# Optimization experiments

Measured on AMD Instinct MI355X. Metric: run time of the kernel, lower is better.

The kernel has to match this reference:

```python
import jax, jax.numpy as jnp
import numpy as np

H, HD, NKV = 16, 128, 4           # heads, head_dim, n_kv_heads (kv_groups=4)
SEL_TOPK, SEL_DIM, SEL_HEADS = 64, 64, 1
ROPE_BASE = 10000.0


def _rope_emb(t, hd):
    inv = 1.0 / (ROPE_BASE ** (jnp.arange(0, hd, 2, dtype=jnp.float32) / hd))
    freqs = jnp.arange(t, dtype=jnp.float32)[:, None] * inv[None, :]
    return jnp.concatenate([freqs, freqs], axis=-1)  # [t, hd]


def _apply_rotary(x, rope):
    # x: [b, t, h, hd]; rope: [t, hd] (rot_dim == hd here)
    cos = jnp.cos(rope)[None, :, None, :]
    sin = jnp.sin(rope)[None, :, None, :]
    x1, x2 = x[..., ::2], x[..., 1::2]
    c, s = cos[..., ::2], sin[..., ::2]
    rot = jnp.stack([x1 * c - x2 * s, x1 * s + x2 * c], axis=-1)
    return rot.reshape(x.shape)


def _selector_mask(q, k):
    # q, k: [b, H, t, hd] in UNrotated form (selector_rope='none'); causal=True
    b, h, t, d = q.shape
    qs = q[:, :SEL_HEADS, :, :SEL_DIM]
    ks = k[:, :SEL_HEADS, :, :SEL_DIM]
    scores = jnp.einsum('bhqd,bhkd->bhqk', qs, ks) / np.sqrt(SEL_DIM).astype(np.float32)
    future = jnp.triu(jnp.ones((t, t), bool), 1)
    scores = jnp.where(future[None, None], -jnp.inf, scores)
    idx = jax.lax.top_k(scores, SEL_TOPK)[1]  # [b, h_sel, t, keep]
    rows = jnp.arange(t)
    scatter_row = lambda im: jnp.zeros((t, t), bool).at[rows[:, None], im].set(True)
    sel = jax.vmap(jax.vmap(scatter_row))(idx)          # [b, h_sel, t, t]
    sel = sel.at[:, :, rows, rows].set(True)            # diagonal always kept
    sel = sel & jnp.tril(jnp.ones((t, t), bool))[None, None]
    sel = jnp.any(sel, axis=1, keepdims=True)           # h_sel < h -> broadcast mask
    return jnp.where(sel, 0.0, -jnp.inf).astype(jnp.float32)


def reference(x, Wq, bq, Wkd, bkd, Wku, bku, Wo, bo):
    b, t, d = x.shape
    G = H // NKV
    q = (x @ Wq + bq).reshape(b, t, H, HD)
    kv = (x @ Wkd + bkd) @ Wku + bku                    # MLA: down then up projection
    k = kv[..., : NKV * HD].reshape(b, t, NKV, HD)
    v = kv[..., NKV * HD:].reshape(b, t, NKV, HD)
    rope = _rope_emb(t, HD)
    qb = _apply_rotary(q, rope).transpose(0, 2, 1, 3)                     # [b,H,t,hd]
    kb = jnp.repeat(_apply_rotary(k, rope).transpose(0, 2, 1, 3), G, 1)   # GQA expand
    vb = jnp.repeat(v.transpose(0, 2, 1, 3), G, 1)
    # selector mask from unrotated q/k, detached (selector_detach=True)
    qu = jax.lax.stop_gradient(q.transpose(0, 2, 1, 3))
    ku = jnp.repeat(jax.lax.stop_gradient(k.transpose(0, 2, 1, 3)), G, 1)
    mask = _selector_mask(qu, ku)                                         # [b,1,t,t]
    scores = jnp.einsum('bhqd,bhkd->bhqk', qb, kb) / np.sqrt(HD).astype(np.float32)
    attn = jax.nn.softmax(scores + mask, axis=-1)
    y = jnp.einsum('bhqk,bhkd->bhqd', attn, vb)
    y = y.transpose(0, 2, 1, 3).reshape(b, t, H * HD)
    return y @ Wo + bo


def setup_inputs() -> dict:
    key = jax.random.key(0)
    ks = jax.random.split(key, 6)
    B, T, D, LAT = 2, 2048, 2048, 512
    s = 0.02
    return {
        'x': jax.random.normal(ks[0], (B, T, D), jnp.float32),
        'Wq': jax.random.normal(ks[1], (D, H * HD), jnp.float32) * s,
        'bq': jnp.zeros((H * HD,), jnp.float32),
        'Wkd': jax.random.normal(ks[2], (D, LAT), jnp.float32) * s,
        'bkd': jnp.zeros((LAT,), jnp.float32),
        'Wku': jax.random.normal(ks[3], (LAT, 2 * NKV * HD), jnp.float32) * s,
        'bku': jnp.zeros((2 * NKV * HD,), jnp.float32),
        'Wo': jax.random.normal(ks[4], (H * HD, D), jnp.float32) * s,
        'bo': jnp.zeros((D,), jnp.float32),
    }
```

## Files before the change

kernel.cpp:

```cpp
#include <hip/hip_runtime.h>

typedef unsigned int u32;
typedef unsigned long long u64;
typedef _Float16 f16;
typedef __attribute__((ext_vector_type(2))) _Float16 f16x2;
typedef __attribute__((ext_vector_type(4))) _Float16 f16x4;
typedef __attribute__((ext_vector_type(8))) _Float16 f16x8;
typedef __attribute__((ext_vector_type(4))) float f32x4;
typedef __attribute__((ext_vector_type(2))) double f64x2;


__device__ __forceinline__ int suX(int jj) { return jj ^ ((jj >> 4) & 7); }

__global__ __launch_bounds__(256) void k_transpose_cast(const float* __restrict__ in,
                                                        f16* __restrict__ out, int R, int C)
{
  __shared__ float tile[32][33];
  int c0 = blockIdx.x * 32, r0 = blockIdx.y * 32;
  int tx = threadIdx.x & 31, ty = threadIdx.x >> 5;
  #pragma unroll
  for (int i = ty; i < 32; i += 8) tile[i][tx] = in[(size_t)(r0 + i) * C + c0 + tx];
  __syncthreads();
  #pragma unroll
  for (int i = ty; i < 32; i += 8) out[(size_t)(c0 + i) * R + r0 + tx] = (f16)tile[tx][i];
}

__global__ __launch_bounds__(256) void k_cast_f16(const float* __restrict__ in,
                                                  f16* __restrict__ out, int n4)
{
  int i = blockIdx.x * 256 + threadIdx.x;
  if (i >= n4) return;
  f32x4 v = *(const f32x4*)&in[(size_t)i * 4];
  f16x4 h; h.x = (f16)v.x; h.y = (f16)v.y; h.z = (f16)v.z; h.w = (f16)v.w;
  *(f16x4*)&out[(size_t)i * 4] = h;
}

__global__ void k_prep_sel(const float* __restrict__ Wq, const float* __restrict__ Wkd,
                           const float* __restrict__ Wku, double* __restrict__ Bsel)
{
  const int k = blockIdx.x;
  const int j = threadIdx.x;
  Bsel[(size_t)k * 128 + j] = (double)Wq[(size_t)k * 2048 + j];
  double s = 0.0;
  for (int l = 0; l < 512; ++l)
    s = fma((double)Wkd[(size_t)k * 512 + l], (double)Wku[(size_t)l * 1024 + j], s);
  Bsel[(size_t)k * 128 + 64 + j] = s;
}

__global__ void k_bias_sel(const float* __restrict__ bq, const float* __restrict__ bkd,
                           const float* __restrict__ Wku, const float* __restrict__ bku,
                           double* __restrict__ bsel)
{
  int j = threadIdx.x;
  if (j < 64) {
    bsel[j] = (double)bq[j];
  } else {
    int jj = j - 64;
    double s = (double)bku[jj];
    for (int l = 0; l < 512; ++l)
      s = fma((double)bkd[l], (double)Wku[(size_t)l * 1024 + jj], s);
    bsel[j] = s;
  }
}

__global__ __launch_bounds__(256) void k_gemm_sel_f64(const float* __restrict__ A,
                                                      const double* __restrict__ Bsel,
                                                      double* __restrict__ partial)
{
  __shared__ double As[32][33];
  __shared__ double Bs[32][66];
  const int m0 = blockIdx.x * 32, n0 = blockIdx.y * 64;
  const int kbase = blockIdx.z * 512, kend = kbase + 512;
  const int tid = threadIdx.x;
  const int tx = tid & 15, ty = tid >> 4;
  const int ar = tid >> 3, ac4 = (tid & 7) * 4;
  double acc[2][4] = {};

  f32x4 aN = *(const f32x4*)&A[(size_t)(m0 + ar) * 2048 + kbase + ac4];
  f64x2 bN[4];
  #pragma unroll
  for (int it = 0; it < 4; ++it) {
    int c = it * 256 + tid; int kk = c >> 5, n2 = (c & 31) * 2;
    bN[it] = *(const f64x2*)&Bsel[(size_t)(kbase + kk) * 128 + n0 + n2];
  }
  for (int k0 = kbase; k0 < kend; k0 += 32) {
    __syncthreads();
    As[ar][ac4] = (double)aN.x; As[ar][ac4 + 1] = (double)aN.y;
    As[ar][ac4 + 2] = (double)aN.z; As[ar][ac4 + 3] = (double)aN.w;
    #pragma unroll
    for (int it = 0; it < 4; ++it) {
      int c = it * 256 + tid; int kk = c >> 5, n2 = (c & 31) * 2;
      Bs[kk][n2] = bN[it].x; Bs[kk][n2 + 1] = bN[it].y;
    }
    __syncthreads();
    if (k0 + 32 < kend) {
      aN = *(const f32x4*)&A[(size_t)(m0 + ar) * 2048 + k0 + 32 + ac4];
      #pragma unroll
      for (int it = 0; it < 4; ++it) {
        int c = it * 256 + tid; int kk = c >> 5, n2 = (c & 31) * 2;
        bN[it] = *(const f64x2*)&Bsel[(size_t)(k0 + 32 + kk) * 128 + n0 + n2];
      }
    }
    #pragma unroll
    for (int kk = 0; kk < 32; ++kk) {
      double a0 = As[ty * 2][kk], a1 = As[ty * 2 + 1][kk];
      f64x2 b01 = *(const f64x2*)&Bs[kk][tx * 4];
      f64x2 b23 = *(const f64x2*)&Bs[kk][tx * 4 + 2];
      acc[0][0] = fma(a0, b01.x, acc[0][0]); acc[0][1] = fma(a0, b01.y, acc[0][1]);
      acc[0][2] = fma(a0, b23.x, acc[0][2]); acc[0][3] = fma(a0, b23.y, acc[0][3]);
      acc[1][0] = fma(a1, b01.x, acc[1][0]); acc[1][1] = fma(a1, b01.y, acc[1][1]);
      acc[1][2] = fma(a1, b23.x, acc[1][2]); acc[1][3] = fma(a1, b23.y, acc[1][3]);
    }
  }
  double* op = partial + (size_t)blockIdx.z * 4096 * 128;
  #pragma unroll
  for (int i = 0; i < 2; ++i) {
    int row = m0 + ty * 2 + i;
    #pragma unroll
    for (int j = 0; j < 4; ++j) {
      int n = n0 + tx * 4 + j;
      op[(size_t)row * 128 + n] = acc[i][j];
    }
  }
}

__global__ __launch_bounds__(256) void k_sel_reduce(const double* __restrict__ partial,
                                                    const double* __restrict__ bias,
                                                    double* __restrict__ qs64,
                                                    double* __restrict__ ks64)
{
  const int idx = blockIdx.x * 256 + threadIdx.x;
  const int row = idx >> 7, n = idx & 127;
  const size_t S = 4096 * 128;
  double v = ((partial[idx] + partial[S + idx]) + partial[2 * S + idx]) + partial[3 * S + idx];
  v += bias[n];
  if (n < 64) qs64[(size_t)row * 64 + n] = v;
  else        ks64[(size_t)row * 64 + (n - 64)] = v;
}

__global__ __launch_bounds__(256) void k_transpose64(const double* __restrict__ in,
                                                     double* __restrict__ out)
{
  __shared__ double tile[32][33];
  const int bt = blockIdx.z;
  const int c0 = blockIdx.x * 32;
  const int r0 = blockIdx.y * 32;
  int tx = threadIdx.x & 31, ty = threadIdx.x >> 5;
  const double* ip = in + (size_t)bt * 2048 * 64;
  double* op = out + (size_t)bt * 64 * 2048;
  #pragma unroll
  for (int i = ty; i < 32; i += 8) tile[i][tx] = ip[(size_t)(r0 + i) * 64 + c0 + tx];
  __syncthreads();
  #pragma unroll
  for (int i = ty; i < 32; i += 8) op[(size_t)(c0 + i) * 2048 + r0 + tx] = tile[tx][i];
}

template <bool OUTF16>
__global__ __launch_bounds__(256) void k_gemm_bt(const f16* __restrict__ A,
                                                 const f16* __restrict__ BT,
                                                 const float* __restrict__ bias,
                                                 float* __restrict__ C, f16* __restrict__ Ch,
                                                 int M, int N, int K, int lda, int ldb, int ldc)
{
  __shared__ __align__(16) f16 As[128 * 64];
  __shared__ __align__(16) f16 Bs[128 * 64];
  const int tid = threadIdx.x;
  const int lane = tid & 63;
  const int wave = tid >> 6;
  int bx = blockIdx.x, by = blockIdx.y;
  {
    const int nwg = gridDim.x * gridDim.y;
    if ((nwg & 7) == 0) {
      const int bid = by * gridDim.x + bx;
      const int cpx = nwg >> 3;
      const int sbid = (bid & 7) * cpx + (bid >> 3);
      bx = sbid % gridDim.x;
      by = sbid / gridDim.x;
    }
  }
  const int m0 = bx * 128, n0 = by * 128;
  const int wr = (wave >> 1) * 64, wc = (wave & 1) * 64;
  const int lrow = lane & 15;
  const int kgrp = (lane >> 4) * 8;
  f32x4 acc[4][4] = {};

  for (int k0 = 0; k0 < K; k0 += 64) {
    __syncthreads();
    #pragma unroll
    for (int it = 0; it < 4; ++it) {
      int c = it * 256 + tid;
      int r = c >> 3, c8 = (c & 7) * 8;
      int lbase = (it * 256 + (tid & 192)) * 8;
      const f16* ga = A + (size_t)(m0 + r) * lda + k0 + c8;
      __builtin_amdgcn_global_load_lds((const __attribute__((address_space(1))) u32*)ga,
                                       (__attribute__((address_space(3))) u32*)&As[lbase],
                                       16, 0, 0);
      const f16* gb = BT + (size_t)(n0 + r) * ldb + k0 + c8;
      __builtin_amdgcn_global_load_lds((const __attribute__((address_space(1))) u32*)gb,
                                       (__attribute__((address_space(3))) u32*)&Bs[lbase],
                                       16, 0, 0);
    }
    __syncthreads();
    #pragma unroll
    for (int ks = 0; ks < 2; ++ks) {
      f16x8 af[4], bfr[4];
      #pragma unroll
      for (int m = 0; m < 4; ++m)
        af[m] = *(const f16x8*)&As[(wr + m * 16 + lrow) * 64 + ks * 32 + kgrp];
      #pragma unroll
      for (int n = 0; n < 4; ++n)
        bfr[n] = *(const f16x8*)&Bs[(wc + n * 16 + lrow) * 64 + ks * 32 + kgrp];
      #pragma unroll
      for (int m = 0; m < 4; ++m)
        #pragma unroll
        for (int n = 0; n < 4; ++n)
          acc[m][n] = __builtin_amdgcn_mfma_f32_16x16x32_f16(af[m], bfr[n], acc[m][n], 0, 0, 0);
    }
  }
  const int rbase = m0 + wr + (lane >> 4) * 4;
  #pragma unroll
  for (int n = 0; n < 4; ++n) {
    int col = n0 + wc + n * 16 + lrow;
    float bv = bias ? bias[col] : 0.0f;
    #pragma unroll
    for (int m = 0; m < 4; ++m) {
      #pragma unroll
      for (int j = 0; j < 4; ++j) {
        int rowi = rbase + m * 16 + j;
        float v = acc[m][n][j] + bv;
        if (OUTF16) Ch[(size_t)rowi * ldc + col] = (f16)v;
        else        C[(size_t)rowi * ldc + col] = v;
      }
    }
  }
}

__global__ void k_rope_table(float* __restrict__ rc, float* __restrict__ rs)
{
  int t = blockIdx.x, i = threadIdx.x;
  int fi = (2 * i) & 63;
  double inv = pow(10000.0, -(double)fi / 64.0);
  double a = (double)t * inv;
  rc[t * 64 + i] = (float)cos(a);
  rs[t * 64 + i] = (float)sin(a);
}

__global__ __launch_bounds__(256) void k_rope_q(const f16* __restrict__ q,
                                                const float* __restrict__ rc,
                                                const float* __restrict__ rs,
                                                f16* __restrict__ out)
{
  int g = blockIdx.x * 256 + threadIdx.x;
  int row = g >> 10, rem = g & 1023;
  int h = rem >> 6, i = rem & 63;
  int t = row & 2047;
  size_t base = (size_t)row * 2048 + h * 128 + 2 * i;
  f16x2 v = *(const f16x2*)&q[base];
  float x1 = (float)v.x, x2 = (float)v.y;
  float c = rc[t * 64 + i], s = rs[t * 64 + i];
  f16x2 o; o.x = (f16)(x1 * c - x2 * s); o.y = (f16)(x1 * s + x2 * c);
  *(f16x2*)&out[base] = o;
}

__global__ __launch_bounds__(256) void k_rope_kv(const f16* __restrict__ kv,
                                                 const float* __restrict__ rc,
                                                 const float* __restrict__ rs,
                                                 f16* __restrict__ kout, f16* __restrict__ vout)
{
  int g = blockIdx.x * 256 + threadIdx.x;
  int row = g >> 8, rem = g & 255;
  int kvh = rem >> 6, i = rem & 63;
  int t = row & 2047;
  size_t kb = (size_t)row * 1024 + kvh * 128 + 2 * i;
  f16x2 kvp = *(const f16x2*)&kv[kb];
  float x1 = (float)kvp.x, x2 = (float)kvp.y;
  float c = rc[t * 64 + i], s = rs[t * 64 + i];
  size_t ob = (size_t)row * 512 + kvh * 128 + 2 * i;
  f16x2 ko; ko.x = (f16)(x1 * c - x2 * s); ko.y = (f16)(x1 * s + x2 * c);
  *(f16x2*)&kout[ob] = ko;
  f16x2 vp = *(const f16x2*)&kv[(size_t)row * 1024 + 512 + kvh * 128 + 2 * i];
  *(f16x2*)&vout[ob] = vp;
}

__global__ __launch_bounds__(256) void k_topk64(const double* __restrict__ qs,
                                                const double* __restrict__ ksT,
                                                int* __restrict__ selcnt,
                                                int* __restrict__ selidx)
{
  const int r0 = blockIdx.x * 2;
  const int b = r0 >> 11;
  const int t0 = r0 & 2047, t1 = t0 + 1;
  const int tid = threadIdx.x;
  if (t1 < 64) {
    for (int lr = 0; lr < 2; ++lr) {
      int t = t0 + lr;
      int* outp = selidx + (size_t)(r0 + lr) * 68;
      for (int jj = tid; jj <= t; jj += 256) outp[jj] = jj;
      if (tid == 0) selcnt[r0 + lr] = t + 1;
    }
    return;
  }
  __shared__ double qrowP[64][2];
  __shared__ u64 su[2][2048];
  __shared__ unsigned hist[256], sA[256], sB[256];
  __shared__ unsigned s_bsel, s_larger, s_cnt;
  __shared__ u64 s_thr;
  __shared__ int s_remfin;
  __shared__ int cand[128];
  __shared__ u64 ckey[128];

  if (tid < 128) qrowP[tid >> 1][tid & 1] = qs[(size_t)(r0 + (tid & 1)) * 64 + (tid >> 1)];
  __syncthreads();
  {
    const double* kb = ksT + (size_t)b * 64 * 2048;
    const int emax = t1 >> 8;
    for (int e = 0; e <= emax; ++e) {
      const int jj = e * 256 + tid;
      double acc0 = 0.0, acc1 = 0.0;
      const double* kp = kb + jj;
      #pragma unroll 16
      for (int d = 0; d < 64; ++d) {
        double kv = kp[(size_t)d * 2048];
        f64x2 qp = *(const f64x2*)&qrowP[d][0];
        acc0 = fma(qp.x, kv, acc0);
        acc1 = fma(qp.y, kv, acc1);
      }
      const int sx = suX(jj);
      u64 u0 = (u64)__double_as_longlong(acc0);
      su[0][sx] = (u0 >> 63) ? ~u0 : (u0 | 0x8000000000000000ull);
      u64 u1 = (u64)__double_as_longlong(acc1);
      su[1][sx] = (u1 >> 63) ? ~u1 : (u1 | 0x8000000000000000ull);
    }
  }
  __syncthreads();

  const int c0 = tid * 8;
  for (int lr = 0; lr < 2; ++lr) {
    const int t = t0 + lr;
    int* outp = selidx + (size_t)(r0 + lr) * 68;
    const u64* S = su[lr];
    u64 prefix = 0;
    int remaining = 64;
    int broke = 0, sh_final = 0;
    for (int byte = 7; byte >= 0; --byte) {
      const int sh = byte * 8;
      hist[tid] = 0;
      __syncthreads();
      {
        unsigned bn[8]; bool vl[8];
        #pragma unroll
        for (int e = 0; e < 8; ++e) {
          int jj = c0 + e;
          u64 u = (jj <= t) ? S[suX(jj)] : 0;
          bool ok = (jj <= t) && ((byte == 7) || (((u ^ prefix) >> (sh + 8)) == 0));
          bn[e] = (unsigned)((u >> sh) & 255);
          vl[e] = ok;
        }
        #pragma unroll
        for (int e = 0; e < 8; ++e) {
          if (vl[e]) {
            bool first = true;
            #pragma unroll
            for (int p = 0; p < 8; ++p)
              if (p < e && vl[p] && bn[p] == bn[e]) first = false;
            if (first) {
              unsigned c = 0;
              #pragma unroll
              for (int q = 0; q < 8; ++q)
                if (q >= e && vl[q] && bn[q] == bn[e]) ++c;
              atomicAdd(&hist[bn[e]], c);
            }
          }
        }
      }
      __syncthreads();
      unsigned* sp = sA; unsigned* dp = sB;
      sp[tid] = hist[tid];
      __syncthreads();
      #pragma unroll
      for (int off = 1; off < 256; off <<= 1) {
        dp[tid] = sp[tid] + ((tid + off < 256) ? sp[tid + off] : 0u);
        __syncthreads();
        unsigned* tpp = sp; sp = dp; dp = tpp;
      }
      unsigned inc = sp[tid];
      unsigned cumAbove = (tid == 255) ? 0u : sp[tid + 1];
      if ((int)cumAbove < remaining && (int)inc >= remaining) {
        s_bsel = (unsigned)tid;
        s_larger = cumAbove;
        s_cnt = inc - cumAbove;
      }
      __syncthreads();
      prefix |= ((u64)s_bsel << sh);
      remaining -= (int)s_larger;
      int cnt = (int)s_cnt;
      __syncthreads();
      if (cnt <= 128) { broke = 1; sh_final = sh; break; }
    }
    u64 thr;
    int remfin;
    if (broke) {
      unsigned cg = 0;
      #pragma unroll
      for (int e = 0; e < 8; ++e) {
        int jj = c0 + e;
        if (jj <= t && (((S[suX(jj)] ^ prefix) >> sh_final) == 0)) ++cg;
      }
      unsigned* sp = sA; unsigned* dp = sB;
      sp[tid] = cg;
      __syncthreads();
      #pragma unroll
      for (int off = 1; off < 256; off <<= 1) {
        dp[tid] = sp[tid] + ((tid >= off) ? sp[tid - off] : 0u);
        __syncthreads();
        unsigned* tpp = sp; sp = dp; dp = tpp;
      }
      const int C = (int)sp[255];
      int pos = (int)(sp[tid] - cg);
      #pragma unroll
      for (int e = 0; e < 8; ++e) {
        int jj = c0 + e;
        if (jj <= t && (((S[suX(jj)] ^ prefix) >> sh_final) == 0)) cand[pos++] = jj;
      }
      __syncthreads();
      if (tid < C) ckey[tid] = S[suX(cand[tid])];
      __syncthreads();
      if (tid < C) {
        u64 k = ckey[tid];
        int g = 0, eq = 0;
        for (int j = 0; j < C; ++j) {
          g += (ckey[j] > k) ? 1 : 0;
          eq += (ckey[j] == k) ? 1 : 0;
        }
        if (g < remaining && remaining <= g + eq) {
          s_thr = k;
          s_remfin = remaining - g;
        }
      }
      __syncthreads();
      thr = s_thr;
      remfin = s_remfin;
    } else {
      thr = prefix;
      remfin = remaining;
    }
    __syncthreads();
    unsigned cg = 0, ct_ = 0;
    #pragma unroll
    for (int e = 0; e < 8; ++e) {
      int jj = c0 + e;
      if (jj <= t) {
        u64 u = S[suX(jj)];
        cg += (u > thr) ? 1u : 0u;
        ct_ += (u == thr) ? 1u : 0u;
      }
    }
    const unsigned pack = cg | (ct_ << 16);
    {
      unsigned* sp = sA; unsigned* dp = sB;
      sp[tid] = pack;
      __syncthreads();
      #pragma unroll
      for (int off = 1; off < 256; off <<= 1) {
        dp[tid] = sp[tid] + ((tid >= off) ? sp[tid - off] : 0u);
        __syncthreads();
        unsigned* tpp = sp; sp = dp; dp = tpp;
      }
      const unsigned excl = sp[tid] - pack;
      const unsigned tot = sp[255];
      const unsigned Gtot = tot & 0xFFFFu;
      const u64 ut = S[suX(t)];
      const unsigned gt = (ut > thr) ? 1u : 0u;
      const unsigned tt = (ut == thr) ? 1u : 0u;
      const int GtotX = (int)(Gtot - gt);
      int gpos = (int)(excl & 0xFFFFu);
      int tpos = (int)(excl >> 16);
      #pragma unroll
      for (int e = 0; e < 8; ++e) {
        int jj = c0 + e;
        if (jj > t) break;
        u64 u = S[suX(jj)];
        if (u > thr) {
          if (jj != t) outp[1 + gpos] = jj;
          ++gpos;
        } else if (u == thr) {
          if (jj != t && tpos < remfin) outp[1 + GtotX + tpos] = jj;
          ++tpos;
        }
      }
      if (tid == 0) {
        outp[0] = t;
        const unsigned Ttot = tot >> 16;
        int tb = (int)(Ttot - tt);
        int emitT = tb < remfin ? tb : remfin;
        selcnt[r0 + lr] = 1 + GtotX + emitT;
      }
    }
    __syncthreads();
  }
}

__global__ __launch_bounds__(256) void k_attn(const f16* __restrict__ qr,
                                              const f16* __restrict__ kr,
                                              const f16* __restrict__ vv,
                                              const int* __restrict__ selcnt,
                                              const int* __restrict__ selidx,
                                              f16* __restrict__ y)
{
  const int blk = blockIdx.x;
  const int row = blk >> 2, kvh = blk & 3;
  const int b = row >> 11;
  const int tid = threadIdx.x, lane = tid & 63, wave = tid >> 6;
  const int cnt = selcnt[row];
  __shared__ int sidx[68];
  __shared__ __align__(16) f16 Kl[65 * 128];
  __shared__ __align__(16) f16 Vl[68 * 128];
  __shared__ f16 qlds[4][128];
  __shared__ __align__(16) float pl[4][68];
  if (tid < cnt) sidx[tid] = selidx[(size_t)row * 68 + tid];
  *(f16x2*)&qlds[wave][lane * 2] =
      *(const f16x2*)&qr[((size_t)row * 16 + kvh * 4 + wave) * 128 + lane * 2];
  __syncthreads();

  const int nch = cnt * 16;
  for (int c = tid; c < nch; c += 256) {
    const int r = c >> 4, ch = c & 15;
    const size_t kbase = ((size_t)(b * 2048 + sidx[r])) * 512 + kvh * 128 + ch * 8;
    f16x8 k8 = *(const f16x8*)&kr[kbase];
    *(f16x8*)&Kl[r * 128 + ((ch ^ (r & 15)) * 8)] = k8;
    f16x8 v8 = *(const f16x8*)&vv[kbase];
    *(f16x8*)&Vl[r * 128 + ch * 8] = v8;
  }
  for (int i = tid; i < (68 - cnt) * 64; i += 256)
    ((u32*)Vl)[cnt * 64 + i] = 0u;
  __syncthreads();

  const float SCALE = 0.08838834764831845f;
  auto dotk = [&](int r) -> float {
    const int sw = r & 15;
    float s = 0.0f;
    #pragma unroll
    for (int i = 0; i < 16; ++i) {
      f16x8 k8 = *(const f16x8*)&Kl[r * 128 + ((i ^ sw) * 8)];
      f16x8 q8 = *(const f16x8*)&qlds[wave][i * 8];
      #pragma unroll
      for (int e = 0; e < 4; ++e) {
        f16x2 ka; ka.x = k8[2 * e]; ka.y = k8[2 * e + 1];
        f16x2 qa; qa.x = q8[2 * e]; qa.y = q8[2 * e + 1];
        s = __builtin_amdgcn_fdot2(ka, qa, s, false);
      }
    }
    return s * SCALE;
  };

  float s1 = -__builtin_inff(), s2 = -__builtin_inff();
  if (lane < cnt) s1 = dotk(lane);
  if (lane + 64 < cnt) s2 = dotk(lane + 64);
  float mx = fmaxf(s1, s2);
  #pragma unroll
  for (int off = 32; off; off >>= 1) mx = fmaxf(mx, __shfl_xor(mx, off));
  float p1 = (lane < cnt) ? __expf(s1 - mx) : 0.0f;
  float p2 = (lane + 64 < cnt) ? __expf(s2 - mx) : 0.0f;
  float l = p1 + p2;
  #pragma unroll
  for (int off = 32; off; off >>= 1) l += __shfl_xor(l, off);
  float linv = 1.0f / l;
  pl[wave][lane] = p1;
  if (lane == 0) pl[wave][64] = p2;
  if (lane < 3) pl[wave][65 + lane] = 0.0f;
  __syncthreads();

  float y0 = 0.0f, y1 = 0.0f;
  const int d2 = lane * 2;
  for (int j = 0; j < cnt; j += 4) {
    f32x4 p4 = *(const f32x4*)&pl[wave][j];
    f16x2 va = *(const f16x2*)&Vl[(j + 0) * 128 + d2];
    f16x2 vb = *(const f16x2*)&Vl[(j + 1) * 128 + d2];
    f16x2 vc = *(const f16x2*)&Vl[(j + 2) * 128 + d2];
    f16x2 vd = *(const f16x2*)&Vl[(j + 3) * 128 + d2];
    y0 = fmaf(p4.x, (float)va.x, y0); y1 = fmaf(p4.x, (float)va.y, y1);
    y0 = fmaf(p4.y, (float)vb.x, y0); y1 = fmaf(p4.y, (float)vb.y, y1);
    y0 = fmaf(p4.z, (float)vc.x, y0); y1 = fmaf(p4.z, (float)vc.y, y1);
    y0 = fmaf(p4.w, (float)vd.x, y0); y1 = fmaf(p4.w, (float)vd.y, y1);
  }
  y0 *= linv; y1 *= linv;
  f16x2 o; o.x = (f16)y0; o.y = (f16)y1;
  *(f16x2*)&y[(size_t)row * 2048 + (kvh * 4 + wave) * 128 + d2] = o;
}

extern "C" void kernel_launch(void* const* d_in, const int* in_sizes, int n_in,
                              void* d_out, int out_size, void* d_ws, size_t ws_size,
                              hipStream_t stream)
{
  (void)in_sizes; (void)n_in; (void)out_size; (void)ws_size;
  const float* x   = (const float*)d_in[0];
  const float* Wq  = (const float*)d_in[1];
  const float* bq  = (const float*)d_in[2];
  const float* Wkd = (const float*)d_in[3];
  const float* bkd = (const float*)d_in[4];
  const float* Wku = (const float*)d_in[5];
  const float* bku = (const float*)d_in[6];
  const float* Wo  = (const float*)d_in[7];
  const float* bo  = (const float*)d_in[8];
  float* out = (float*)d_out;

  char* ws = (char*)d_ws;
  size_t o = 0;
  auto alloc = [&](size_t bytes) -> void* {
    o = (o + 255) & ~(size_t)255;
    void* p = ws + o;
    o += bytes;
    return p;
  };
  f16* WqT   = (f16*)alloc(2048ull * 2048 * 2);
  f16* WoT   = (f16*)alloc(2048ull * 2048 * 2);
  f16* WkdT  = (f16*)alloc(512ull * 2048 * 2);
  f16* WkuT  = (f16*)alloc(1024ull * 512 * 2);
  f16* xh    = (f16*)alloc(4096ull * 2048 * 2);
  f16* qmain = (f16*)alloc(4096ull * 2048 * 2);
  f16* kvh_  = (f16*)alloc(4096ull * 1024 * 2);
  f16* cbf   = (f16*)alloc(4096ull * 512 * 2);
  float* rc  = (float*)alloc(2048ull * 64 * 4);
  float* rs  = (float*)alloc(2048ull * 64 * 4);
  f16* qrope = (f16*)alloc(4096ull * 2048 * 2);
  f16* krope = (f16*)alloc(4096ull * 512 * 2);
  f16* vbf   = (f16*)alloc(4096ull * 512 * 2);
  int* selcnt = (int*)alloc(4096ull * 4);
  int* selidx = (int*)alloc(4096ull * 68 * 4);
  double* Bsel = (double*)alloc(2048ull * 128 * 8);
  double* bsel = (double*)alloc(128 * 8);
  double* qs64 = (double*)alloc(4096ull * 64 * 8);
  double* ks64 = (double*)alloc(4096ull * 64 * 8);
  double* ksT  = (double*)alloc(2ull * 64 * 2048 * 8);
  f16* yh = qmain;
  double* partial = (double*)qrope;

  k_transpose_cast<<<dim3(64, 64), 256, 0, stream>>>(Wq, WqT, 2048, 2048);
  k_transpose_cast<<<dim3(16, 64), 256, 0, stream>>>(Wkd, WkdT, 2048, 512);
  k_transpose_cast<<<dim3(32, 16), 256, 0, stream>>>(Wku, WkuT, 512, 1024);
  k_transpose_cast<<<dim3(64, 64), 256, 0, stream>>>(Wo, WoT, 2048, 2048);
  k_cast_f16<<<8192, 256, 0, stream>>>(x, xh, 2097152);

  k_prep_sel<<<2048, 64, 0, stream>>>(Wq, Wkd, Wku, Bsel);
  k_bias_sel<<<1, 128, 0, stream>>>(bq, bkd, Wku, bku, bsel);
  k_gemm_sel_f64<<<dim3(128, 2, 4), 256, 0, stream>>>(x, Bsel, partial);
  k_sel_reduce<<<2048, 256, 0, stream>>>(partial, bsel, qs64, ks64);
  k_transpose64<<<dim3(2, 64, 2), 256, 0, stream>>>(ks64, ksT);

  k_gemm_bt<true><<<dim3(32, 16), 256, 0, stream>>>(xh, WqT, bq, nullptr, qmain,
                                                    4096, 2048, 2048, 2048, 2048, 2048);
  k_gemm_bt<true><<<dim3(32, 4), 256, 0, stream>>>(xh, WkdT, bkd, nullptr, cbf,
                                                   4096, 512, 2048, 2048, 2048, 512);
  k_gemm_bt<true><<<dim3(32, 8), 256, 0, stream>>>(cbf, WkuT, bku, nullptr, kvh_,
                                                   4096, 1024, 512, 512, 512, 1024);

  k_rope_table<<<2048, 64, 0, stream>>>(rc, rs);
  k_rope_q<<<16384, 256, 0, stream>>>(qmain, rc, rs, qrope);
  k_rope_kv<<<4096, 256, 0, stream>>>(kvh_, rc, rs, krope, vbf);

  k_topk64<<<2048, 256, 0, stream>>>(qs64, ksT, selcnt, selidx);

  k_attn<<<16384, 256, 0, stream>>>(qrope, krope, vbf, selcnt, selidx, yh);

  k_gemm_bt<false><<<dim3(32, 16), 256, 0, stream>>>(yh, WoT, bo, out, nullptr,
                                                     4096, 2048, 2048, 2048, 2048, 2048);
}
```

Measured before the change: 547.1 us.

## Fuse RoPE into projection GEMM epilogues and streamline sparse attention gather

Applies rotary embedding directly in the Q and KV-up GEMM epilogues, using lane shuffles to pair adjacent columns, and splits K/V outputs there. This removes the separate rope kernels and their full read/write passes over q and kv. The attention kernel now issues all K/V gather loads into registers before writing shared memory, and it stores probabilities as f16 so the PV product can use fdot2. The f16 probabilities lower precision, and the epilogue adds per-element cos/sin table loads.

```diff
diff --git a/kernel.cpp b/kernel.cpp
--- a/kernel.cpp
+++ b/kernel.cpp
@@ -155,11 +155,14 @@
   for (int i = ty; i < 32; i += 8) op[(size_t)(c0 + i) * 2048 + r0 + tx] = tile[tx][i];
 }
 
-template <bool OUTF16>
+template <int MODE>
 __global__ __launch_bounds__(256) void k_gemm_bt(const f16* __restrict__ A,
                                                  const f16* __restrict__ BT,
                                                  const float* __restrict__ bias,
                                                  float* __restrict__ C, f16* __restrict__ Ch,
+                                                 f16* __restrict__ Kout, f16* __restrict__ Vout,
+                                                 const float* __restrict__ rc,
+                                                 const float* __restrict__ rs,
                                                  int M, int N, int K, int lda, int ldb, int ldc)
 {
   __shared__ __align__(16) f16 As[128 * 64];
@@ -222,14 +225,34 @@
   for (int n = 0; n < 4; ++n) {
     int col = n0 + wc + n * 16 + lrow;
     float bv = bias ? bias[col] : 0.0f;
+    const int ri = (col & 127) >> 1;
     #pragma unroll
     for (int m = 0; m < 4; ++m) {
       #pragma unroll
       for (int j = 0; j < 4; ++j) {
         int rowi = rbase + m * 16 + j;
         float v = acc[m][n][j] + bv;
-        if (OUTF16) Ch[(size_t)rowi * ldc + col] = (f16)v;
-        else        C[(size_t)rowi * ldc + col] = v;
+        if (MODE == 0) {
+          C[(size_t)rowi * ldc + col] = v;
+        } else if (MODE == 1) {
+          Ch[(size_t)rowi * ldc + col] = (f16)v;
+        } else if (MODE == 2) {
+          float vp = __shfl_xor(v, 1);
+          int t = rowi & 2047;
+          float c_ = rc[t * 64 + ri], s_ = rs[t * 64 + ri];
+          float r_ = (lrow & 1) ? (vp * s_ + v * c_) : (v * c_ - vp * s_);
+          Ch[(size_t)rowi * ldc + col] = (f16)r_;
+        } else {
+          float vp = __shfl_xor(v, 1);
+          if (n0 < 512) {
+            int t = rowi & 2047;
+            float c_ = rc[t * 64 + ri], s_ = rs[t * 64 + ri];
+            float r_ = (lrow & 1) ? (vp * s_ + v * c_) : (v * c_ - vp * s_);
+            Kout[(size_t)rowi * 512 + col] = (f16)r_;
+          } else {
+            Vout[(size_t)rowi * 512 + (col - 512)] = (f16)v;
+          }
+        }
       }
     }
   }
@@ -243,43 +266,6 @@
   double a = (double)t * inv;
   rc[t * 64 + i] = (float)cos(a);
   rs[t * 64 + i] = (float)sin(a);
-}
-
-__global__ __launch_bounds__(256) void k_rope_q(const f16* __restrict__ q,
-                                                const float* __restrict__ rc,
-                                                const float* __restrict__ rs,
-                                                f16* __restrict__ out)
-{
-  int g = blockIdx.x * 256 + threadIdx.x;
-  int row = g >> 10, rem = g & 1023;
-  int h = rem >> 6, i = rem & 63;
-  int t = row & 2047;
-  size_t base = (size_t)row * 2048 + h * 128 + 2 * i;
-  f16x2 v = *(const f16x2*)&q[base];
-  float x1 = (float)v.x, x2 = (float)v.y;
-  float c = rc[t * 64 + i], s = rs[t * 64 + i];
-  f16x2 o; o.x = (f16)(x1 * c - x2 * s); o.y = (f16)(x1 * s + x2 * c);
-  *(f16x2*)&out[base] = o;
-}
-
-__global__ __launch_bounds__(256) void k_rope_kv(const f16* __restrict__ kv,
-                                                 const float* __restrict__ rc,
-                                                 const float* __restrict__ rs,
-                                                 f16* __restrict__ kout, f16* __restrict__ vout)
-{
-  int g = blockIdx.x * 256 + threadIdx.x;
-  int row = g >> 8, rem = g & 255;
-  int kvh = rem >> 6, i = rem & 63;
-  int t = row & 2047;
-  size_t kb = (size_t)row * 1024 + kvh * 128 + 2 * i;
-  f16x2 kvp = *(const f16x2*)&kv[kb];
-  float x1 = (float)kvp.x, x2 = (float)kvp.y;
-  float c = rc[t * 64 + i], s = rs[t * 64 + i];
-  size_t ob = (size_t)row * 512 + kvh * 128 + 2 * i;
-  f16x2 ko; ko.x = (f16)(x1 * c - x2 * s); ko.y = (f16)(x1 * s + x2 * c);
-  *(f16x2*)&kout[ob] = ko;
-  f16x2 vp = *(const f16x2*)&kv[(size_t)row * 1024 + 512 + kvh * 128 + 2 * i];
-  *(f16x2*)&vout[ob] = vp;
 }
 
 __global__ __launch_bounds__(256) void k_topk64(const double* __restrict__ qs,
@@ -516,20 +502,31 @@
   __shared__ __align__(16) f16 Kl[65 * 128];
   __shared__ __align__(16) f16 Vl[68 * 128];
   __shared__ f16 qlds[4][128];
-  __shared__ __align__(16) float pl[4][68];
+  __shared__ __align__(4) f16 ph[4][72];
   if (tid < cnt) sidx[tid] = selidx[(size_t)row * 68 + tid];
   *(f16x2*)&qlds[wave][lane * 2] =
       *(const f16x2*)&qr[((size_t)row * 16 + kvh * 4 + wave) * 128 + lane * 2];
   __syncthreads();
 
-  const int nch = cnt * 16;
-  for (int c = tid; c < nch; c += 256) {
+  f16x8 kreg[5], vreg[5];
+  int rr[5], cc[5]; bool vld[5];
+  #pragma unroll
+  for (int it = 0; it < 5; ++it) {
+    const int c = it * 256 + tid;
     const int r = c >> 4, ch = c & 15;
-    const size_t kbase = ((size_t)(b * 2048 + sidx[r])) * 512 + kvh * 128 + ch * 8;
-    f16x8 k8 = *(const f16x8*)&kr[kbase];
-    *(f16x8*)&Kl[r * 128 + ((ch ^ (r & 15)) * 8)] = k8;
-    f16x8 v8 = *(const f16x8*)&vv[kbase];
-    *(f16x8*)&Vl[r * 128 + ch * 8] = v8;
+    const bool ok = (r < cnt);
+    const int rsafe = ok ? sidx[r] : sidx[0];
+    const size_t kbase = ((size_t)(b * 2048 + rsafe)) * 512 + kvh * 128 + ch * 8;
+    kreg[it] = *(const f16x8*)&kr[kbase];
+    vreg[it] = *(const f16x8*)&vv[kbase];
+    rr[it] = r; cc[it] = ch; vld[it] = ok;
+  }
+  #pragma unroll
+  for (int it = 0; it < 5; ++it) {
+    if (vld[it]) {
+      *(f16x8*)&Kl[rr[it] * 128 + ((cc[it] ^ (rr[it] & 15)) * 8)] = kreg[it];
+      *(f16x8*)&Vl[rr[it] * 128 + cc[it] * 8] = vreg[it];
+    }
   }
   for (int i = tid; i < (68 - cnt) * 64; i += 256)
     ((u32*)Vl)[cnt * 64 + i] = 0u;
@@ -565,23 +562,21 @@
   #pragma unroll
   for (int off = 32; off; off >>= 1) l += __shfl_xor(l, off);
   float linv = 1.0f / l;
-  pl[wave][lane] = p1;
-  if (lane == 0) pl[wave][64] = p2;
-  if (lane < 3) pl[wave][65 + lane] = 0.0f;
+  ph[wave][lane] = (f16)p1;
+  if (lane == 0) ph[wave][64] = (f16)p2;
+  if (lane >= 1 && lane < 8) ph[wave][64 + lane] = (f16)0.f;
   __syncthreads();
 
   float y0 = 0.0f, y1 = 0.0f;
   const int d2 = lane * 2;
-  for (int j = 0; j < cnt; j += 4) {
-    f32x4 p4 = *(const f32x4*)&pl[wave][j];
+  for (int j = 0; j < cnt; j += 2) {
+    f16x2 pp = *(const f16x2*)&ph[wave][j];
     f16x2 va = *(const f16x2*)&Vl[(j + 0) * 128 + d2];
     f16x2 vb = *(const f16x2*)&Vl[(j + 1) * 128 + d2];
-    f16x2 vc = *(const f16x2*)&Vl[(j + 2) * 128 + d2];
-    f16x2 vd = *(const f16x2*)&Vl[(j + 3) * 128 + d2];
-    y0 = fmaf(p4.x, (float)va.x, y0); y1 = fmaf(p4.x, (float)va.y, y1);
-    y0 = fmaf(p4.y, (float)vb.x, y0); y1 = fmaf(p4.y, (float)vb.y, y1);
-    y0 = fmaf(p4.z, (float)vc.x, y0); y1 = fmaf(p4.z, (float)vc.y, y1);
-    y0 = fmaf(p4.w, (float)vd.x, y0); y1 = fmaf(p4.w, (float)vd.y, y1);
+    f16x2 v0; v0.x = va.x; v0.y = vb.x;
+    f16x2 v1; v1.x = va.y; v1.y = vb.y;
+    y0 = __builtin_amdgcn_fdot2(pp, v0, y0, false);
+    y1 = __builtin_amdgcn_fdot2(pp, v1, y1, false);
   }
   y0 *= linv; y1 *= linv;
   f16x2 o; o.x = (f16)y0; o.y = (f16)y1;
@@ -617,8 +612,7 @@
   f16* WkdT  = (f16*)alloc(512ull * 2048 * 2);
   f16* WkuT  = (f16*)alloc(1024ull * 512 * 2);
   f16* xh    = (f16*)alloc(4096ull * 2048 * 2);
-  f16* qmain = (f16*)alloc(4096ull * 2048 * 2);
-  f16* kvh_  = (f16*)alloc(4096ull * 1024 * 2);
+  f16* yh    = (f16*)alloc(4096ull * 2048 * 2);
   f16* cbf   = (f16*)alloc(4096ull * 512 * 2);
   float* rc  = (float*)alloc(2048ull * 64 * 4);
   float* rs  = (float*)alloc(2048ull * 64 * 4);
@@ -632,7 +626,6 @@
   double* qs64 = (double*)alloc(4096ull * 64 * 8);
   double* ks64 = (double*)alloc(4096ull * 64 * 8);
   double* ksT  = (double*)alloc(2ull * 64 * 2048 * 8);
-  f16* yh = qmain;
   double* partial = (double*)qrope;
 
   k_transpose_cast<<<dim3(64, 64), 256, 0, stream>>>(Wq, WqT, 2048, 2048);
@@ -640,6 +633,7 @@
   k_transpose_cast<<<dim3(32, 16), 256, 0, stream>>>(Wku, WkuT, 512, 1024);
   k_transpose_cast<<<dim3(64, 64), 256, 0, stream>>>(Wo, WoT, 2048, 2048);
   k_cast_f16<<<8192, 256, 0, stream>>>(x, xh, 2097152);
+  k_rope_table<<<2048, 64, 0, stream>>>(rc, rs);
 
   k_prep_sel<<<2048, 64, 0, stream>>>(Wq, Wkd, Wku, Bsel);
   k_bias_sel<<<1, 128, 0, stream>>>(bq, bkd, Wku, bku, bsel);
@@ -647,21 +641,21 @@
   k_sel_reduce<<<2048, 256, 0, stream>>>(partial, bsel, qs64, ks64);
   k_transpose64<<<dim3(2, 64, 2), 256, 0, stream>>>(ks64, ksT);
 
-  k_gemm_bt<true><<<dim3(32, 16), 256, 0, stream>>>(xh, WqT, bq, nullptr, qmain,
-                                                    4096, 2048, 2048, 2048, 2048, 2048);
-  k_gemm_bt<true><<<dim3(32, 4), 256, 0, stream>>>(xh, WkdT, bkd, nullptr, cbf,
-                                                   4096, 512, 2048, 2048, 2048, 512);
-  k_gemm_bt<true><<<dim3(32, 8), 256, 0, stream>>>(cbf, WkuT, bku, nullptr, kvh_,
-                                                   4096, 1024, 512, 512, 512, 1024);
-
-  k_rope_table<<<2048, 64, 0, stream>>>(rc, rs);
-  k_rope_q<<<16384, 256, 0, stream>>>(qmain, rc, rs, qrope);
-  k_rope_kv<<<4096, 256, 0, stream>>>(kvh_, rc, rs, krope, vbf);
+  k_gemm_bt<2><<<dim3(32, 16), 256, 0, stream>>>(xh, WqT, bq, nullptr, qrope,
+                                                 nullptr, nullptr, rc, rs,
+                                                 4096, 2048, 2048, 2048, 2048, 2048);
+  k_gemm_bt<1><<<dim3(32, 4), 256, 0, stream>>>(xh, WkdT, bkd, nullptr, cbf,
+                                                nullptr, nullptr, nullptr, nullptr,
+                                                4096, 512, 2048, 2048, 2048, 512);
+  k_gemm_bt<3><<<dim3(32, 8), 256, 0, stream>>>(cbf, WkuT, bku, nullptr, nullptr,
+                                                krope, vbf, rc, rs,
+                                                4096, 1024, 512, 512, 512, 1024);
 
   k_topk64<<<2048, 256, 0, stream>>>(qs64, ksT, selcnt, selidx);
 
   k_attn<<<16384, 256, 0, stream>>>(qrope, krope, vbf, selcnt, selidx, yh);
 
-  k_gemm_bt<false><<<dim3(32, 16), 256, 0, stream>>>(yh, WoT, bo, out, nullptr,
-                                                     4096, 2048, 2048, 2048, 2048, 2048);
-}
+  k_gemm_bt<0><<<dim3(32, 16), 256, 0, stream>>>(yh, WoT, bo, out, nullptr,
+                                                 nullptr, nullptr, nullptr, nullptr,
+                                                 4096, 2048, 2048, 2048, 2048, 2048);
+}
```

New measurement: 542.4 us. No clear change (-0.9%).
